# Performance work log

Hardware: AMD Instinct MI355X
Metric: run time of the kernel (lower is better)

## Reference

```python
import jax, jax.numpy as jnp
import numpy as np

B, S, H, E, K = 4, 4096, 1024, 8, 2


def setup_inputs() -> dict:
    key = jax.random.key(0)
    ks = jax.random.split(key, 5)
    scale = 1.0 / np.sqrt(H)
    return {
        "x": jax.random.normal(ks[0], (B, S, H), dtype=jnp.float32),
        "gate_w": jax.random.normal(ks[1], (H, E), dtype=jnp.float32) * scale,
        "gate_b": jnp.zeros((E,), dtype=jnp.float32),
        "expert_w": jax.random.normal(ks[2], (E, H, H), dtype=jnp.float32) * scale,
        "expert_b": jnp.zeros((E, H), dtype=jnp.float32),
    }


def reference(x, gate_w, gate_b, expert_w, expert_b):
    bsz, seq_len, hsz = x.shape
    h = x.reshape(-1, hsz)                              # [T, H], T = B*S

    # --- router ---
    router_logits = h @ gate_w + gate_b                 # [T, E]
    probs = jax.nn.softmax(router_logits, axis=-1)
    top_w, top_idx = jax.lax.top_k(probs, K)            # [T, K]
    top_w = top_w / jnp.sum(top_w, axis=-1, keepdims=True)

    # combine weight per (token, expert): sum over top-k slots of w * onehot(idx)
    one_hot = jax.nn.one_hot(top_idx, E, dtype=h.dtype)  # [T, K, E]
    combine = jnp.einsum("tk,tke->te", top_w, one_hot)   # [T, E]

    # --- experts (dense grouped GEMM, masked-combined; same math as gather/scatter loop) ---
    expert_out = jnp.einsum("th,ehd->etd", h, expert_w) + expert_b[:, None, :]  # [E, T, H]
    out = jnp.einsum("te,etd->td", combine, expert_out)                          # [T, H]

    return out.reshape(bsz, seq_len, hsz), router_logits
```

## Files before the change

### kernel.cpp

```cpp
#include <hip/hip_runtime.h>

#define TT 16384
#define HH 1024
#define EE 8

typedef __attribute__((ext_vector_type(8))) short short8;
typedef __attribute__((ext_vector_type(4))) float f32x4;

__device__ inline unsigned short f2bf(float f) {
    union { float f; unsigned int u; } v; v.f = f;
    unsigned int u = v.u;
    unsigned int r = (u + 0x7FFFu + ((u >> 16) & 1u)) >> 16;
    return (unsigned short)r;
}

__global__ __launch_bounds__(256) void transpose_w_kernel(
    const float* __restrict__ w, unsigned short* __restrict__ wt)
{
    __shared__ unsigned short tile[64][66];
    int bid = blockIdx.x;
    int e   = bid >> 8;
    int rem = bid & 255;
    int hb  = ((rem >> 4) & 15) * 64;
    int db  = (rem & 15) * 64;
    int tid = threadIdx.x;
    int c4  = (tid & 15) * 4;
    int r0  = tid >> 4;

    const float* we = w + (size_t)e * HH * HH;
    #pragma unroll
    for (int i = 0; i < 4; ++i) {
        int r = i * 16 + r0;
        float4 v = *(const float4*)(we + (size_t)(hb + r) * HH + db + c4);
        tile[r][c4 + 0] = f2bf(v.x);
        tile[r][c4 + 1] = f2bf(v.y);
        tile[r][c4 + 2] = f2bf(v.z);
        tile[r][c4 + 3] = f2bf(v.w);
    }
    __syncthreads();
    unsigned short* wte = wt + (size_t)e * HH * HH;
    #pragma unroll
    for (int i = 0; i < 4; ++i) {
        int dr = i * 16 + r0;
        ushort4 o;
        o.x = tile[c4 + 0][dr];
        o.y = tile[c4 + 1][dr];
        o.z = tile[c4 + 2][dr];
        o.w = tile[c4 + 3][dr];
        *(ushort4*)(wte + (size_t)(db + dr) * HH + hb + c4) = o;
    }
}

__global__ __launch_bounds__(256) void router_logits_kernel(
    const float* __restrict__ x, const float* __restrict__ gw,
    const float* __restrict__ gb, float* __restrict__ logits,
    int* __restrict__ tops_i, float* __restrict__ tops_w)
{
    __shared__ float gwt[EE][HH];
    int tid = threadIdx.x;
    for (int i = tid; i < (HH * EE) / 4; i += 256) {
        float4 v = ((const float4*)gw)[i];
        int b4 = i * 4;
        gwt[(b4 + 0) & 7][(b4 + 0) >> 3] = v.x;
        gwt[(b4 + 1) & 7][(b4 + 1) >> 3] = v.y;
        gwt[(b4 + 2) & 7][(b4 + 2) >> 3] = v.z;
        gwt[(b4 + 3) & 7][(b4 + 3) >> 3] = v.w;
    }
    __syncthreads();

    const int lane = tid & 63;
    const int wv   = tid >> 6;
    const int t    = blockIdx.x * 4 + wv;
    const float* xrow = x + (size_t)t * HH;

    float4 v0 = *(const float4*)(xrow + 0 * 256 + lane * 4);
    float4 v1 = *(const float4*)(xrow + 1 * 256 + lane * 4);
    float4 v2 = *(const float4*)(xrow + 2 * 256 + lane * 4);
    float4 v3 = *(const float4*)(xrow + 3 * 256 + lane * 4);

    float acc[8];
    #pragma unroll
    for (int e = 0; e < 8; ++e) {
        float4 g0 = *(const float4*)(&gwt[e][0 * 256 + lane * 4]);
        float4 g1 = *(const float4*)(&gwt[e][1 * 256 + lane * 4]);
        float4 g2 = *(const float4*)(&gwt[e][2 * 256 + lane * 4]);
        float4 g3 = *(const float4*)(&gwt[e][3 * 256 + lane * 4]);
        acc[e] = v0.x * g0.x + v0.y * g0.y + v0.z * g0.z + v0.w * g0.w
               + v1.x * g1.x + v1.y * g1.y + v1.z * g1.z + v1.w * g1.w
               + v2.x * g2.x + v2.y * g2.y + v2.z * g2.z + v2.w * g2.w
               + v3.x * g3.x + v3.y * g3.y + v3.z * g3.z + v3.w * g3.w;
    }
    #pragma unroll
    for (int e = 0; e < 8; ++e) {
        #pragma unroll
        for (int off = 32; off >= 1; off >>= 1)
            acc[e] += __shfl_xor(acc[e], off, 64);
    }
    float lg[8];
    #pragma unroll
    for (int e = 0; e < 8; ++e) lg[e] = acc[e] + gb[e];

    float myv = 0.0f;
    #pragma unroll
    for (int e = 0; e < 8; ++e) myv = (lane == e) ? lg[e] : myv;
    if (lane < 8) logits[(size_t)t * EE + lane] = myv;

    int i0 = 0;
    #pragma unroll
    for (int e = 1; e < 8; ++e) if (lg[e] > lg[i0]) i0 = e;
    int i1 = (i0 == 0) ? 1 : 0;
    #pragma unroll
    for (int e = 0; e < 8; ++e) if (e != i0 && lg[e] > lg[i1]) i1 = e;

    float w0 = 1.0f / (1.0f + expf(lg[i1] - lg[i0]));

    if (lane == 0) {
        tops_i[t] = i0 | (i1 << 3);
        tops_w[t] = w0;
    }
}

__global__ __launch_bounds__(256) void build_lists_kernel(
    const int* __restrict__ tops_i, const float* __restrict__ tops_w,
    int* __restrict__ counts, int* __restrict__ tokl, float* __restrict__ wl)
{
    __shared__ int lcnt[EE];
    __shared__ int gbase[EE];
    int tid = threadIdx.x;
    if (tid < EE) lcnt[tid] = 0;
    __syncthreads();

    int t   = blockIdx.x * 256 + tid;
    int rec = tops_i[t];
    int i0  = rec & 7;
    int i1  = (rec >> 3) & 7;
    float w0 = tops_w[t];
    float w1 = 1.0f - w0;

    int r0 = atomicAdd(&lcnt[i0], 1);
    int r1 = atomicAdd(&lcnt[i1], 1);
    __syncthreads();

    if (tid < EE) gbase[tid] = atomicAdd(&counts[tid], lcnt[tid]);
    __syncthreads();

    int p0 = gbase[i0] + r0;
    tokl[i0 * TT + p0] = t; wl[i0 * TT + p0] = w0;
    int p1 = gbase[i1] + r1;
    tokl[i1 * TT + p1] = t; wl[i1 * TT + p1] = w1;
}

__global__ __launch_bounds__(256) void stream_init_kernel(
    const float* __restrict__ x, const float* __restrict__ eb,
    const int* __restrict__ tops_i, const float* __restrict__ tops_w,
    unsigned short* __restrict__ xb, float* __restrict__ out)
{
    const int N4 = TT * HH / 4;
    int stride = gridDim.x * 256;
    for (int f = blockIdx.x * 256 + threadIdx.x; f < N4; f += stride) {
        int t  = f >> 8;
        int c4 = f & 255;
        int rec = tops_i[t];
        int i0  = rec & 7;
        int i1  = (rec >> 3) & 7;
        float w0 = tops_w[t];
        float w1 = 1.0f - w0;

        float4 v = ((const float4*)x)[f];
        ushort4 bv;
        bv.x = f2bf(v.x); bv.y = f2bf(v.y); bv.z = f2bf(v.z); bv.w = f2bf(v.w);
        ((ushort4*)xb)[f] = bv;

        float4 a = *(const float4*)(eb + (size_t)i0 * HH + c4 * 4);
        float4 c = *(const float4*)(eb + (size_t)i1 * HH + c4 * 4);
        float4 r;
        r.x = w0 * a.x + w1 * c.x;
        r.y = w0 * a.y + w1 * c.y;
        r.z = w0 * a.z + w1 * c.z;
        r.w = w0 * a.w + w1 * c.w;
        ((float4*)out)[f] = r;
    }
}

#define BM 128
#define BN 128
#define BK 32
#define NT (HH / BK)

__global__ __launch_bounds__(256) void moe_gemm_kernel(
    const unsigned short* __restrict__ xb, const unsigned short* __restrict__ wt,
    const int* __restrict__ counts, const int* __restrict__ tokl,
    const float* __restrict__ wl, float* __restrict__ out)
{
    int bid = blockIdx.x;
    int e   = bid & 7;
    int j   = bid >> 3;
    int mb  = j >> 3;
    int nb  = j & 7;
    int cnt = counts[e];
    int row0 = mb * BM;
    if (row0 >= cnt) return;

    __shared__ __align__(16) unsigned short Alds[2][BM * BK];
    __shared__ __align__(16) unsigned short Blds[2][BN * BK];
    __shared__ int   toks[BM];
    __shared__ float wgts[BM];

    int tid = threadIdx.x;
    if (tid < BM) {
        int g = row0 + tid;
        bool ok = g < cnt;
        toks[tid] = ok ? tokl[e * TT + g] : 0;
        wgts[tid] = ok ? wl[e * TT + g] : 0.0f;
    }
    __syncthreads();

    const int lane = tid & 63;
    const int wv   = tid >> 6;
    const int wr   = wv >> 1, wc = wv & 1;
    const int mrow = wr * 64, ncol = wc * 64;

    f32x4 acc[4][4];
    #pragma unroll
    for (int m = 0; m < 4; ++m)
        #pragma unroll
        for (int n = 0; n < 4; ++n) acc[m][n] = (f32x4)0.0f;

    const unsigned short* wte = wt + (size_t)e * HH * HH + (size_t)(nb * BN) * HH;

    const int srow = tid >> 2;
    const int scol = (tid & 3) * 8;
    const unsigned short* abase0 = xb + (size_t)toks[srow] * HH + scol;
    const unsigned short* abase1 = xb + (size_t)toks[srow + 64] * HH + scol;
    const unsigned short* bbase0 = wte + (size_t)srow * HH + scol;
    const unsigned short* bbase1 = wte + (size_t)(srow + 64) * HH + scol;
    const int ldst = tid * 16;

#define STAGE(buf, k0)                                                         \
    {                                                                          \
        __builtin_amdgcn_global_load_lds(                                      \
            (const __attribute__((address_space(1))) void*)(abase0 + (k0)),    \
            (__attribute__((address_space(3))) void*)((char*)&Alds[buf][0] + ldst), \
            16, 0, 0);                                                         \
        __builtin_amdgcn_global_load_lds(                                      \
            (const __attribute__((address_space(1))) void*)(abase1 + (k0)),    \
            (__attribute__((address_space(3))) void*)((char*)&Alds[buf][0] + ldst + 4096), \
            16, 0, 0);                                                         \
        __builtin_amdgcn_global_load_lds(                                      \
            (const __attribute__((address_space(1))) void*)(bbase0 + (k0)),    \
            (__attribute__((address_space(3))) void*)((char*)&Blds[buf][0] + ldst), \
            16, 0, 0);                                                         \
        __builtin_amdgcn_global_load_lds(                                      \
            (const __attribute__((address_space(1))) void*)(bbase1 + (k0)),    \
            (__attribute__((address_space(3))) void*)((char*)&Blds[buf][0] + ldst + 4096), \
            16, 0, 0);                                                         \
    }

#define COMPUTE(buf)                                                           \
    {                                                                          \
        int kb = (lane >> 4) * 16;                                             \
        short8 av[4], bv[4];                                                   \
        _Pragma("unroll")                                                      \
        for (int m = 0; m < 4; ++m)                                            \
            av[m] = *(const short8*)((const char*)&Alds[buf][0] + (mrow + m * 16 + (lane & 15)) * 64 + kb); \
        _Pragma("unroll")                                                      \
        for (int n = 0; n < 4; ++n)                                            \
            bv[n] = *(const short8*)((const char*)&Blds[buf][0] + (ncol + n * 16 + (lane & 15)) * 64 + kb); \
        _Pragma("unroll")                                                      \
        for (int m = 0; m < 4; ++m)                                            \
            _Pragma("unroll")                                                  \
            for (int n = 0; n < 4; ++n)                                        \
                acc[m][n] = __builtin_amdgcn_mfma_f32_16x16x32_bf16(av[m], bv[n], acc[m][n], 0, 0, 0); \
    }

    STAGE(0, 0);

    for (int kt = 0; kt < NT - 1; kt += 2) {
        STAGE(1, (kt + 1) * BK);
        asm volatile("s_waitcnt vmcnt(4)" ::: "memory");
        __builtin_amdgcn_sched_barrier(0);
        __builtin_amdgcn_s_barrier();
        __builtin_amdgcn_sched_barrier(0);
        COMPUTE(0);
        __builtin_amdgcn_sched_barrier(0);
        __builtin_amdgcn_s_barrier();
        __builtin_amdgcn_sched_barrier(0);
        if (kt + 2 < NT) {
            STAGE(0, (kt + 2) * BK);
            asm volatile("s_waitcnt vmcnt(4)" ::: "memory");
        } else {
            asm volatile("s_waitcnt vmcnt(0)" ::: "memory");
        }
        __builtin_amdgcn_sched_barrier(0);
        __builtin_amdgcn_s_barrier();
        __builtin_amdgcn_sched_barrier(0);
        COMPUTE(1);
        __builtin_amdgcn_sched_barrier(0);
        __builtin_amdgcn_s_barrier();
        __builtin_amdgcn_sched_barrier(0);
    }
    {
        asm volatile("s_waitcnt vmcnt(0)" ::: "memory");
        __builtin_amdgcn_sched_barrier(0);
    }

#undef STAGE
#undef COMPUTE

    #pragma unroll
    for (int m = 0; m < 4; ++m) {
        int lr0 = mrow + m * 16 + ((lane >> 4) << 2);
        #pragma unroll
        for (int rg = 0; rg < 4; ++rg) {
            int lr = lr0 + rg;
            int tkn = toks[lr];
            float wg = wgts[lr];
            if (wg != 0.0f) {
                float* orow = out + (size_t)tkn * HH + nb * BN + ncol + (lane & 15);
                #pragma unroll
                for (int n = 0; n < 4; ++n)
                    atomicAdd(orow + n * 16, wg * acc[m][n][rg]);
            }
        }
    }
}

extern "C" void kernel_launch(void* const* d_in, const int* in_sizes, int n_in,
                              void* d_out, int out_size, void* d_ws, size_t ws_size,
                              hipStream_t stream) {
    const float* x  = (const float*)d_in[0];
    const float* gw = (const float*)d_in[1];
    const float* gb = (const float*)d_in[2];
    const float* ew = (const float*)d_in[3];
    const float* eb = (const float*)d_in[4];
    float* out    = (float*)d_out;
    float* logits = out + (size_t)TT * HH;

    char* w = (char*)d_ws;
    unsigned short* xb = (unsigned short*)w;
    unsigned short* wt = (unsigned short*)(w + (size_t)TT * HH * 2);
    char* p  = w + (size_t)TT * HH * 2 + (size_t)EE * HH * HH * 2;
    int*   counts = (int*)p;
    int*   tokl   = (int*)(p + 256);
    float* wl     = (float*)(p + 256 + (size_t)EE * TT * 4);
    int*   tops_i = (int*)(p + 256 + 2 * (size_t)EE * TT * 4);
    float* tops_w = (float*)(p + 256 + 2 * (size_t)EE * TT * 4 + TT * 4);

    hipMemsetAsync(counts, 0, 256, stream);
    hipLaunchKernelGGL(transpose_w_kernel, dim3(EE * 256), dim3(256), 0, stream, ew, wt);
    hipLaunchKernelGGL(router_logits_kernel, dim3(TT / 4), dim3(256), 0, stream,
                       x, gw, gb, logits, tops_i, tops_w);
    hipLaunchKernelGGL(build_lists_kernel, dim3(TT / 256), dim3(256), 0, stream,
                       tops_i, tops_w, counts, tokl, wl);
    hipLaunchKernelGGL(stream_init_kernel, dim3(2048), dim3(256), 0, stream,
                       x, eb, tops_i, tops_w, xb, out);
    hipLaunchKernelGGL(moe_gemm_kernel, dim3(EE * (TT / BM) * (HH / BN)), dim3(256), 0, stream,
                       xb, wt, counts, tokl, wl, out);
}
```

Measured before the change: 333.4 us.

## Merge prep kernels into fewer launches and XOR-swizzle GEMM LDS tiles

The weight transpose and the router kernel become one launch that splits work by block index. List building and the bf16 stream/init pass are merged into a second launch, which removes two kernel launches and their idle gaps. Separately, the GEMM's LDS staging and fragment reads now use an XOR swizzle on the 16-byte k-chunks to reduce bank conflicts. The combined prep kernel now reserves 32KB of shared memory even for the transpose blocks, which may lower occupancy for that phase.

```diff
diff --git a/kernel.cpp b/kernel.cpp
--- a/kernel.cpp
+++ b/kernel.cpp
@@ -14,150 +14,149 @@
     return (unsigned short)r;
 }
 
-__global__ __launch_bounds__(256) void transpose_w_kernel(
-    const float* __restrict__ w, unsigned short* __restrict__ wt)
-{
-    __shared__ unsigned short tile[64][66];
-    int bid = blockIdx.x;
-    int e   = bid >> 8;
-    int rem = bid & 255;
-    int hb  = ((rem >> 4) & 15) * 64;
-    int db  = (rem & 15) * 64;
-    int tid = threadIdx.x;
-    int c4  = (tid & 15) * 4;
-    int r0  = tid >> 4;
-
-    const float* we = w + (size_t)e * HH * HH;
-    #pragma unroll
-    for (int i = 0; i < 4; ++i) {
-        int r = i * 16 + r0;
-        float4 v = *(const float4*)(we + (size_t)(hb + r) * HH + db + c4);
-        tile[r][c4 + 0] = f2bf(v.x);
-        tile[r][c4 + 1] = f2bf(v.y);
-        tile[r][c4 + 2] = f2bf(v.z);
-        tile[r][c4 + 3] = f2bf(v.w);
-    }
-    __syncthreads();
-    unsigned short* wte = wt + (size_t)e * HH * HH;
-    #pragma unroll
-    for (int i = 0; i < 4; ++i) {
-        int dr = i * 16 + r0;
-        ushort4 o;
-        o.x = tile[c4 + 0][dr];
-        o.y = tile[c4 + 1][dr];
-        o.z = tile[c4 + 2][dr];
-        o.w = tile[c4 + 3][dr];
-        *(ushort4*)(wte + (size_t)(db + dr) * HH + hb + c4) = o;
-    }
-}
-
-__global__ __launch_bounds__(256) void router_logits_kernel(
+__global__ __launch_bounds__(256) void prep_kernel(
+    const float* __restrict__ ew, unsigned short* __restrict__ wt,
     const float* __restrict__ x, const float* __restrict__ gw,
     const float* __restrict__ gb, float* __restrict__ logits,
     int* __restrict__ tops_i, float* __restrict__ tops_w)
 {
-    __shared__ float gwt[EE][HH];
+    __shared__ __align__(16) char smem[EE * HH * 4];
     int tid = threadIdx.x;
-    for (int i = tid; i < (HH * EE) / 4; i += 256) {
-        float4 v = ((const float4*)gw)[i];
-        int b4 = i * 4;
-        gwt[(b4 + 0) & 7][(b4 + 0) >> 3] = v.x;
-        gwt[(b4 + 1) & 7][(b4 + 1) >> 3] = v.y;
-        gwt[(b4 + 2) & 7][(b4 + 2) >> 3] = v.z;
-        gwt[(b4 + 3) & 7][(b4 + 3) >> 3] = v.w;
-    }
-    __syncthreads();
-
-    const int lane = tid & 63;
-    const int wv   = tid >> 6;
-    const int t    = blockIdx.x * 4 + wv;
-    const float* xrow = x + (size_t)t * HH;
-
-    float4 v0 = *(const float4*)(xrow + 0 * 256 + lane * 4);
-    float4 v1 = *(const float4*)(xrow + 1 * 256 + lane * 4);
-    float4 v2 = *(const float4*)(xrow + 2 * 256 + lane * 4);
-    float4 v3 = *(const float4*)(xrow + 3 * 256 + lane * 4);
-
-    float acc[8];
-    #pragma unroll
-    for (int e = 0; e < 8; ++e) {
-        float4 g0 = *(const float4*)(&gwt[e][0 * 256 + lane * 4]);
-        float4 g1 = *(const float4*)(&gwt[e][1 * 256 + lane * 4]);
-        float4 g2 = *(const float4*)(&gwt[e][2 * 256 + lane * 4]);
-        float4 g3 = *(const float4*)(&gwt[e][3 * 256 + lane * 4]);
-        acc[e] = v0.x * g0.x + v0.y * g0.y + v0.z * g0.z + v0.w * g0.w
-               + v1.x * g1.x + v1.y * g1.y + v1.z * g1.z + v1.w * g1.w
-               + v2.x * g2.x + v2.y * g2.y + v2.z * g2.z + v2.w * g2.w
-               + v3.x * g3.x + v3.y * g3.y + v3.z * g3.z + v3.w * g3.w;
-    }
-    #pragma unroll
-    for (int e = 0; e < 8; ++e) {
-        #pragma unroll
-        for (int off = 32; off >= 1; off >>= 1)
-            acc[e] += __shfl_xor(acc[e], off, 64);
-    }
-    float lg[8];
-    #pragma unroll
-    for (int e = 0; e < 8; ++e) lg[e] = acc[e] + gb[e];
-
-    float myv = 0.0f;
-    #pragma unroll
-    for (int e = 0; e < 8; ++e) myv = (lane == e) ? lg[e] : myv;
-    if (lane < 8) logits[(size_t)t * EE + lane] = myv;
-
-    int i0 = 0;
-    #pragma unroll
-    for (int e = 1; e < 8; ++e) if (lg[e] > lg[i0]) i0 = e;
-    int i1 = (i0 == 0) ? 1 : 0;
-    #pragma unroll
-    for (int e = 0; e < 8; ++e) if (e != i0 && lg[e] > lg[i1]) i1 = e;
-
-    float w0 = 1.0f / (1.0f + expf(lg[i1] - lg[i0]));
-
-    if (lane == 0) {
-        tops_i[t] = i0 | (i1 << 3);
-        tops_w[t] = w0;
-    }
-}
-
-__global__ __launch_bounds__(256) void build_lists_kernel(
-    const int* __restrict__ tops_i, const float* __restrict__ tops_w,
-    int* __restrict__ counts, int* __restrict__ tokl, float* __restrict__ wl)
-{
-    __shared__ int lcnt[EE];
-    __shared__ int gbase[EE];
-    int tid = threadIdx.x;
-    if (tid < EE) lcnt[tid] = 0;
-    __syncthreads();
-
-    int t   = blockIdx.x * 256 + tid;
-    int rec = tops_i[t];
-    int i0  = rec & 7;
-    int i1  = (rec >> 3) & 7;
-    float w0 = tops_w[t];
-    float w1 = 1.0f - w0;
-
-    int r0 = atomicAdd(&lcnt[i0], 1);
-    int r1 = atomicAdd(&lcnt[i1], 1);
-    __syncthreads();
-
-    if (tid < EE) gbase[tid] = atomicAdd(&counts[tid], lcnt[tid]);
-    __syncthreads();
-
-    int p0 = gbase[i0] + r0;
-    tokl[i0 * TT + p0] = t; wl[i0 * TT + p0] = w0;
-    int p1 = gbase[i1] + r1;
-    tokl[i1 * TT + p1] = t; wl[i1 * TT + p1] = w1;
-}
-
-__global__ __launch_bounds__(256) void stream_init_kernel(
+
+    if (blockIdx.x < 2048) {
+        unsigned short (*tile)[66] = (unsigned short(*)[66])smem;
+        int bid = blockIdx.x;
+        int e   = bid >> 8;
+        int rem = bid & 255;
+        int hb  = ((rem >> 4) & 15) * 64;
+        int db  = (rem & 15) * 64;
+        int c4  = (tid & 15) * 4;
+        int r0  = tid >> 4;
+
+        const float* we = ew + (size_t)e * HH * HH;
+        #pragma unroll
+        for (int i = 0; i < 4; ++i) {
+            int r = i * 16 + r0;
+            float4 v = *(const float4*)(we + (size_t)(hb + r) * HH + db + c4);
+            tile[r][c4 + 0] = f2bf(v.x);
+            tile[r][c4 + 1] = f2bf(v.y);
+            tile[r][c4 + 2] = f2bf(v.z);
+            tile[r][c4 + 3] = f2bf(v.w);
+        }
+        __syncthreads();
+        unsigned short* wte = wt + (size_t)e * HH * HH;
+        #pragma unroll
+        for (int i = 0; i < 4; ++i) {
+            int dr = i * 16 + r0;
+            ushort4 o;
+            o.x = tile[c4 + 0][dr];
+            o.y = tile[c4 + 1][dr];
+            o.z = tile[c4 + 2][dr];
+            o.w = tile[c4 + 3][dr];
+            *(ushort4*)(wte + (size_t)(db + dr) * HH + hb + c4) = o;
+        }
+    } else {
+        float (*gwt)[HH] = (float(*)[HH])smem;
+        for (int i = tid; i < (HH * EE) / 4; i += 256) {
+            float4 v = ((const float4*)gw)[i];
+            int b4 = i * 4;
+            gwt[(b4 + 0) & 7][(b4 + 0) >> 3] = v.x;
+            gwt[(b4 + 1) & 7][(b4 + 1) >> 3] = v.y;
+            gwt[(b4 + 2) & 7][(b4 + 2) >> 3] = v.z;
+            gwt[(b4 + 3) & 7][(b4 + 3) >> 3] = v.w;
+        }
+        __syncthreads();
+
+        const int lane = tid & 63;
+        const int wv   = tid >> 6;
+        const int t    = (blockIdx.x - 2048) * 4 + wv;
+        const float* xrow = x + (size_t)t * HH;
+
+        float4 v0 = *(const float4*)(xrow + 0 * 256 + lane * 4);
+        float4 v1 = *(const float4*)(xrow + 1 * 256 + lane * 4);
+        float4 v2 = *(const float4*)(xrow + 2 * 256 + lane * 4);
+        float4 v3 = *(const float4*)(xrow + 3 * 256 + lane * 4);
+
+        float acc[8];
+        #pragma unroll
+        for (int e = 0; e < 8; ++e) {
+            float4 g0 = *(const float4*)(&gwt[e][0 * 256 + lane * 4]);
+            float4 g1 = *(const float4*)(&gwt[e][1 * 256 + lane * 4]);
+            float4 g2 = *(const float4*)(&gwt[e][2 * 256 + lane * 4]);
+            float4 g3 = *(const float4*)(&gwt[e][3 * 256 + lane * 4]);
+            acc[e] = v0.x * g0.x + v0.y * g0.y + v0.z * g0.z + v0.w * g0.w
+                   + v1.x * g1.x + v1.y * g1.y + v1.z * g1.z + v1.w * g1.w
+                   + v2.x * g2.x + v2.y * g2.y + v2.z * g2.z + v2.w * g2.w
+                   + v3.x * g3.x + v3.y * g3.y + v3.z * g3.z + v3.w * g3.w;
+        }
+        #pragma unroll
+        for (int e = 0; e < 8; ++e) {
+            #pragma unroll
+            for (int off = 32; off >= 1; off >>= 1)
+                acc[e] += __shfl_xor(acc[e], off, 64);
+        }
+        float lg[8];
+        #pragma unroll
+        for (int e = 0; e < 8; ++e) lg[e] = acc[e] + gb[e];
+
+        float myv = 0.0f;
+        #pragma unroll
+        for (int e = 0; e < 8; ++e) myv = (lane == e) ? lg[e] : myv;
+        if (lane < 8) logits[(size_t)t * EE + lane] = myv;
+
+        int i0 = 0;
+        #pragma unroll
+        for (int e = 1; e < 8; ++e) if (lg[e] > lg[i0]) i0 = e;
+        int i1 = (i0 == 0) ? 1 : 0;
+        #pragma unroll
+        for (int e = 0; e < 8; ++e) if (e != i0 && lg[e] > lg[i1]) i1 = e;
+
+        float w0 = 1.0f / (1.0f + expf(lg[i1] - lg[i0]));
+
+        if (lane == 0) {
+            tops_i[t] = i0 | (i1 << 3);
+            tops_w[t] = w0;
+        }
+    }
+}
+
+__global__ __launch_bounds__(256) void stream_lists_kernel(
     const float* __restrict__ x, const float* __restrict__ eb,
     const int* __restrict__ tops_i, const float* __restrict__ tops_w,
+    int* __restrict__ counts, int* __restrict__ tokl, float* __restrict__ wl,
     unsigned short* __restrict__ xb, float* __restrict__ out)
 {
+    int tid = threadIdx.x;
+
+    if (blockIdx.x < TT / 256) {
+        __shared__ int lcnt[EE];
+        __shared__ int gbase[EE];
+        if (tid < EE) lcnt[tid] = 0;
+        __syncthreads();
+
+        int t   = blockIdx.x * 256 + tid;
+        int rec = tops_i[t];
+        int i0  = rec & 7;
+        int i1  = (rec >> 3) & 7;
+        float w0 = tops_w[t];
+        float w1 = 1.0f - w0;
+
+        int r0 = atomicAdd(&lcnt[i0], 1);
+        int r1 = atomicAdd(&lcnt[i1], 1);
+        __syncthreads();
+
+        if (tid < EE) gbase[tid] = atomicAdd(&counts[tid], lcnt[tid]);
+        __syncthreads();
+
+        int p0 = gbase[i0] + r0;
+        tokl[i0 * TT + p0] = t; wl[i0 * TT + p0] = w0;
+        int p1 = gbase[i1] + r1;
+        tokl[i1 * TT + p1] = t; wl[i1 * TT + p1] = w1;
+    }
+
     const int N4 = TT * HH / 4;
     int stride = gridDim.x * 256;
-    for (int f = blockIdx.x * 256 + threadIdx.x; f < N4; f += stride) {
+    for (int f = blockIdx.x * 256 + tid; f < N4; f += stride) {
         int t  = f >> 8;
         int c4 = f & 255;
         int rec = tops_i[t];
@@ -228,8 +227,9 @@
 
     const unsigned short* wte = wt + (size_t)e * HH * HH + (size_t)(nb * BN) * HH;
 
-    const int srow = tid >> 2;
-    const int scol = (tid & 3) * 8;
+    const int srow  = tid >> 2;
+    const int schk  = (tid & 3) ^ (srow & 3);
+    const int scol  = schk * 8;
     const unsigned short* abase0 = xb + (size_t)toks[srow] * HH + scol;
     const unsigned short* abase1 = xb + (size_t)toks[srow + 64] * HH + scol;
     const unsigned short* bbase0 = wte + (size_t)srow * HH + scol;
@@ -256,16 +256,17 @@
             16, 0, 0);                                                         \
     }
 
+    const int rchk = ((lane >> 4) ^ (lane & 3)) * 16;
+
 #define COMPUTE(buf)                                                           \
     {                                                                          \
-        int kb = (lane >> 4) * 16;                                             \
         short8 av[4], bv[4];                                                   \
         _Pragma("unroll")                                                      \
         for (int m = 0; m < 4; ++m)                                            \
-            av[m] = *(const short8*)((const char*)&Alds[buf][0] + (mrow + m * 16 + (lane & 15)) * 64 + kb); \
+            av[m] = *(const short8*)((const char*)&Alds[buf][0] + (mrow + m * 16 + (lane & 15)) * 64 + rchk); \
         _Pragma("unroll")                                                      \
         for (int n = 0; n < 4; ++n)                                            \
-            bv[n] = *(const short8*)((const char*)&Blds[buf][0] + (ncol + n * 16 + (lane & 15)) * 64 + kb); \
+            bv[n] = *(const short8*)((const char*)&Blds[buf][0] + (ncol + n * 16 + (lane & 15)) * 64 + rchk); \
         _Pragma("unroll")                                                      \
         for (int m = 0; m < 4; ++m)                                            \
             _Pragma("unroll")                                                  \
@@ -299,10 +300,8 @@
         __builtin_amdgcn_s_barrier();
         __builtin_amdgcn_sched_barrier(0);
     }
-    {
-        asm volatile("s_waitcnt vmcnt(0)" ::: "memory");
-        __builtin_amdgcn_sched_barrier(0);
-    }
+    asm volatile("s_waitcnt vmcnt(0)" ::: "memory");
+    __builtin_amdgcn_sched_barrier(0);
 
 #undef STAGE
 #undef COMPUTE
@@ -347,13 +346,10 @@
     float* tops_w = (float*)(p + 256 + 2 * (size_t)EE * TT * 4 + TT * 4);
 
     hipMemsetAsync(counts, 0, 256, stream);
-    hipLaunchKernelGGL(transpose_w_kernel, dim3(EE * 256), dim3(256), 0, stream, ew, wt);
-    hipLaunchKernelGGL(router_logits_kernel, dim3(TT / 4), dim3(256), 0, stream,
-                       x, gw, gb, logits, tops_i, tops_w);
-    hipLaunchKernelGGL(build_lists_kernel, dim3(TT / 256), dim3(256), 0, stream,
-                       tops_i, tops_w, counts, tokl, wl);
-    hipLaunchKernelGGL(stream_init_kernel, dim3(2048), dim3(256), 0, stream,
-                       x, eb, tops_i, tops_w, xb, out);
+    hipLaunchKernelGGL(prep_kernel, dim3(2048 + TT / 4), dim3(256), 0, stream,
+                       ew, wt, x, gw, gb, logits, tops_i, tops_w);
+    hipLaunchKernelGGL(stream_lists_kernel, dim3(2048), dim3(256), 0, stream,
+                       x, eb, tops_i, tops_w, counts, tokl, wl, xb, out);
     hipLaunchKernelGGL(moe_gemm_kernel, dim3(EE * (TT / BM) * (HH / BN)), dim3(256), 0, stream,
                        xb, wt, counts, tokl, wl, out);
 }
```

After: 327.2 us. No clear change (-1.9%).
